# Kernel tuning notes

Hardware: AMD Instinct MI355X
Metric: run time of the kernel (lower is better)

## Reference

```python
import jax, jax.numpy as jnp
import numpy as np

WIDTH = 1024
NUM_HEADS = 8
POWER = 8.0
MIN_RAD, MAX_RAD = 0.9, 0.999


def setup_inputs() -> dict:
    key = jax.random.key(0)
    k_x, k_a, k_wi, k_wa = jax.random.split(key, 4)
    B, L, W, H = 4, 8192, WIDTH, NUM_HEADS
    bw = W // H
    x = jax.random.normal(k_x, (B, L, W), dtype=jnp.float32)
    # a_param init, matching RGLRU.__init__
    unif = jax.random.uniform(k_a, shape=(W,))
    a_real = 0.5 * jnp.log(unif * (MAX_RAD**2 - MIN_RAD**2) + MIN_RAD**2 + 1e-08)
    a_param = jnp.log(jnp.exp(-a_real) - 1.0)
    scale = jnp.sqrt(1.0 / bw).astype(jnp.float32)
    w_in = jax.random.normal(k_wi, (H, bw, bw), dtype=jnp.float32) * scale
    b_in = jnp.zeros((H, bw), dtype=jnp.float32)
    w_a = jax.random.normal(k_wa, (H, bw, bw), dtype=jnp.float32) * scale
    b_a = jnp.zeros((H, bw), dtype=jnp.float32)
    return {"x": x, "a_param": a_param, "w_in": w_in, "b_in": b_in,
            "w_a": w_a, "b_a": b_a}


def _block_diag_linear(x, w, b):
    # x: [B, L, W]; w: [H, bw, bw]; b: [H, bw]
    B, L, W = x.shape
    H, bw, _ = w.shape
    xh = x.reshape(B, L, H, bw)
    y = jnp.einsum('blhi,hij->blhj', xh, w) + b
    return y.reshape(B, L, W)


def reference(x, a_param, w_in, b_in, w_a, b_a):
    gate_x = jax.nn.sigmoid(_block_diag_linear(x, w_in, b_in))
    gate_a = jax.nn.sigmoid(_block_diag_linear(x, w_a, b_a))
    log_a = -POWER * gate_a * jax.nn.softplus(a_param)          # [B, L, W]
    a = jnp.exp(log_a)
    a_squared = jnp.exp(2.0 * log_a)
    normalized_x = x * gate_x * jnp.sqrt(1.0 - a_squared)        # [B, L, W]

    h0 = jnp.zeros_like(normalized_x[:, 0, :])                   # [B, W]

    def step(h, inp):
        a_t, x_t = inp                                           # [B, W] each
        h = a_t * h + x_t
        return h, h

    # scan over time axis: move L to leading dim
    _, ys = jax.lax.scan(step, h0,
                         (jnp.swapaxes(a, 0, 1), jnp.swapaxes(normalized_x, 0, 1)))
    return jnp.swapaxes(ys, 0, 1)                                # [B, L, W]
```

## Files before the change

kernel.cpp:

```cpp
#include <hip/hip_runtime.h>
#include <math.h>

#define NB 4
#define NL 8192
#define NW 1024
#define NH 8
#define BWID 128
#define POWERF 8.0f

#define TM 64
#define NRC (NL / TM)
#define NCHAIN (NB * NH)
#define NBLK (NRC * NCHAIN)

typedef __attribute__((ext_vector_type(8))) short bf16x8;
typedef __attribute__((ext_vector_type(8))) unsigned short u16x8;
typedef __attribute__((ext_vector_type(4))) float f32x4;

__device__ __forceinline__ unsigned short bf_hi(float f) {
  return (unsigned short)(__float_as_uint(f) >> 16);
}
__device__ __forceinline__ float bf_f(unsigned short h) {
  return __uint_as_float(((unsigned)h) << 16);
}

__global__ void prep_kernel(const float* __restrict__ w_in,
                            const float* __restrict__ w_a,
                            const float* __restrict__ a_param,
                            unsigned short* __restrict__ wt,
                            float* __restrict__ sp,
                            unsigned long long* __restrict__ hcarry,
                            int* __restrict__ ticket) {
  const int gtid = blockIdx.x * 256 + threadIdx.x;
  const int k   = gtid & 127;
  const int col = (gtid >> 7) & 127;
  const int hh  = (gtid >> 14) & 7;
  const int mat = gtid >> 17;
  const float* src = mat ? w_a : w_in;
  const float v = src[((size_t)hh * 128 + k) * 128 + col];
  const unsigned short hi = bf_hi(v);
  const unsigned short lo = bf_hi(v - bf_f(hi));
  wt[(((size_t)(mat * 2 + 0) * 8 + hh) * 128 + col) * 128 + k] = hi;
  wt[(((size_t)(mat * 2 + 1) * 8 + hh) * 128 + col) * 128 + k] = lo;
  if (gtid < NW) sp[gtid] = log1pf(expf(a_param[gtid]));
  const size_t ci = (size_t)gtid * 2;
  hcarry[ci] = 0ull;
  hcarry[ci + 1] = 0ull;
  if (gtid == 0) *ticket = 0;
}

__global__ __launch_bounds__(256, 3)
void fused_kernel(const float* __restrict__ x,
                  const unsigned short* __restrict__ wt,
                  const float* __restrict__ sp,
                  const float* __restrict__ b_in,
                  const float* __restrict__ b_a,
                  float* __restrict__ out,
                  int* __restrict__ ticket,
                  unsigned long long* __restrict__ hcarry) {
  __shared__ char smem[49152];
  char* const pXh = smem;
  char* const pXl = smem + 16384;
  char* const pW  = smem + 32768;
  char* const pSeg = smem + 32768;

  const int tid  = threadIdx.x;
  if (tid == 0) *(int*)smem = atomicAdd(ticket, 1);
  __syncthreads();
  const int vbid = *(const int*)smem;
  __syncthreads();
  const int rc = vbid >> 5;
  const int bh = vbid & 31;
  const int b  = bh >> 3;
  const int h  = bh & 7;

  const int lane = tid & 63;
  const int wid  = tid >> 6;
  const int g  = lane >> 4;
  const int ln = lane & 15;
  const int wr = wid >> 1;
  const int wc = wid & 1;

  const size_t xbase = ((size_t)b * NL + (size_t)rc * TM) * NW + h * BWID;

  int wsoff[4], wdoff[4];
#pragma unroll
  for (int i = 0; i < 4; ++i) {
    const int chunk = tid + 256 * i;
    const int split = chunk >> 9;
    const int rem = chunk & 511;
    const int col = rem >> 2;
    const int kk8 = (rem & 3) * 8;
    wsoff[i] = split * 131072 + h * 16384 + col * 128 + kk8;
    wdoff[i] = col * 128 + ((split * 64 + kk8 * 2) ^ ((col & 7) << 4));
  }
  u16x8 wreg[4];
#pragma unroll
  for (int i = 0; i < 4; ++i) wreg[i] = *(const u16x8*)(wt + wsoff[i]);

#pragma unroll
  for (int i = 0; i < 4; ++i) {
    const int chunk = tid + 256 * i;
    const int row = chunk >> 4;
    const int k8  = (chunk & 15) * 8;
    const float4 v0 = *(const float4*)(x + xbase + (size_t)row * NW + k8);
    const float4 v1 = *(const float4*)(x + xbase + (size_t)row * NW + k8 + 4);
    const float f[8] = {v0.x, v0.y, v0.z, v0.w, v1.x, v1.y, v1.z, v1.w};
    u16x8 vh, vl;
#pragma unroll
    for (int j = 0; j < 8; ++j) {
      const unsigned short hi = bf_hi(f[j]);
      vh[j] = hi;
      vl[j] = bf_hi(f[j] - bf_f(hi));
    }
    const int off = row * 256 + ((k8 * 2) ^ ((row & 15) << 4));
    *(u16x8*)(pXh + off) = vh;
    *(u16x8*)(pXl + off) = vl;
  }
  __syncthreads();
#pragma unroll
  for (int i = 0; i < 4; ++i) *(u16x8*)(pW + wdoff[i]) = wreg[i];
#pragma unroll
  for (int i = 0; i < 4; ++i)
    wreg[i] = *(const u16x8*)(wt + wsoff[i] + 262144);

  f32x4 accx[2][4], acca[2][4];
#pragma unroll
  for (int rt = 0; rt < 2; ++rt)
#pragma unroll
    for (int ct = 0; ct < 4; ++ct) {
      accx[rt][ct] = (f32x4){0.f, 0.f, 0.f, 0.f};
      acca[rt][ct] = (f32x4){0.f, 0.f, 0.f, 0.f};
    }

  const int csw = (ln & 7) << 4;
  const int gk  = g * 16;

#pragma unroll 1
  for (int j = 0; j < 4; ++j) {
    const int kt = j * 32;
    __syncthreads();
    bf16x8 Ah[2], Al[2];
#pragma unroll
    for (int rt = 0; rt < 2; ++rt) {
      const int arow = wr * 32 + rt * 16 + ln;
      const int abyte = arow * 256 + (((kt + g * 8) * 2) ^ ((arow & 15) << 4));
      Ah[rt] = *(const bf16x8*)(pXh + abyte);
      Al[rt] = *(const bf16x8*)(pXl + abyte);
    }
#pragma unroll
    for (int ct = 0; ct < 4; ++ct) {
      const int cb = (wc * 64 + ct * 16 + ln) * 128;
      const bf16x8 Bh = *(const bf16x8*)(pW + cb + ((gk) ^ csw));
      const bf16x8 Bl = *(const bf16x8*)(pW + cb + ((64 + gk) ^ csw));
#pragma unroll
      for (int rt = 0; rt < 2; ++rt) {
        accx[rt][ct] = __builtin_amdgcn_mfma_f32_16x16x32_bf16(Ah[rt], Bh, accx[rt][ct], 0, 0, 0);
        accx[rt][ct] = __builtin_amdgcn_mfma_f32_16x16x32_bf16(Al[rt], Bh, accx[rt][ct], 0, 0, 0);
        accx[rt][ct] = __builtin_amdgcn_mfma_f32_16x16x32_bf16(Ah[rt], Bl, accx[rt][ct], 0, 0, 0);
      }
    }
    __syncthreads();
#pragma unroll
    for (int i = 0; i < 4; ++i) *(u16x8*)(pW + wdoff[i]) = wreg[i];
    if (j < 3) {
#pragma unroll
      for (int i = 0; i < 4; ++i)
        wreg[i] = *(const u16x8*)(wt + wsoff[i] + kt + 32);
    }
    __syncthreads();
#pragma unroll
    for (int ct = 0; ct < 4; ++ct) {
      const int cb = (wc * 64 + ct * 16 + ln) * 128;
      const bf16x8 Bh = *(const bf16x8*)(pW + cb + ((gk) ^ csw));
      const bf16x8 Bl = *(const bf16x8*)(pW + cb + ((64 + gk) ^ csw));
#pragma unroll
      for (int rt = 0; rt < 2; ++rt) {
        acca[rt][ct] = __builtin_amdgcn_mfma_f32_16x16x32_bf16(Ah[rt], Bh, acca[rt][ct], 0, 0, 0);
        acca[rt][ct] = __builtin_amdgcn_mfma_f32_16x16x32_bf16(Al[rt], Bh, acca[rt][ct], 0, 0, 0);
        acca[rt][ct] = __builtin_amdgcn_mfma_f32_16x16x32_bf16(Ah[rt], Bl, acca[rt][ct], 0, 0, 0);
      }
    }
    __syncthreads();
    if (j < 3) {
#pragma unroll
      for (int i = 0; i < 4; ++i) *(u16x8*)(pW + wdoff[i]) = wreg[i];
#pragma unroll
      for (int i = 0; i < 4; ++i)
        wreg[i] = *(const u16x8*)(wt + wsoff[i] + 262144 + kt + 32);
    }
  }

  float av_sav[2][4][4], xn_sav[2][4][4];
#pragma unroll
  for (int ct = 0; ct < 4; ++ct) {
    const int col = wc * 64 + ct * 16 + ln;
    const float bi  = b_in[h * BWID + col];
    const float ba  = b_a[h * BWID + col];
    const float spv = sp[h * BWID + col];
#pragma unroll
    for (int rt = 0; rt < 2; ++rt) {
#pragma unroll
      for (int r = 0; r < 4; ++r) {
        const int row = wr * 32 + rt * 16 + g * 4 + r;
        const float zx = accx[rt][ct][r] + bi;
        const float za = acca[rt][ct][r] + ba;
        const int xoff = row * 256 + ((col * 2) ^ ((row & 15) << 4));
        const float xv = bf_f(*(const unsigned short*)(pXh + xoff)) +
                         bf_f(*(const unsigned short*)(pXl + xoff));
        const float gx = __builtin_amdgcn_rcpf(1.f + __expf(-zx));
        const float ga = __builtin_amdgcn_rcpf(1.f + __expf(-za));
        const float la = -POWERF * ga * spv;
        const float av = __expf(la);
        const float asq = __expf(2.f * la);
        av_sav[rt][ct][r] = av;
        xn_sav[rt][ct][r] = xv * gx * sqrtf(fmaxf(1.f - asq, 0.f));
      }
    }
  }

#pragma unroll
  for (int ct = 0; ct < 4; ++ct) {
    const int col = wc * 64 + ct * 16 + ln;
#pragma unroll
    for (int rt = 0; rt < 2; ++rt) {
      float A4 = 1.f, h4 = 0.f;
#pragma unroll
      for (int r = 0; r < 4; ++r) {
        h4 = fmaf(av_sav[rt][ct][r], h4, xn_sav[rt][ct][r]);
        A4 *= av_sav[rt][ct][r];
      }
      const int s = wr * 8 + rt * 4 + g;
      *(float2*)(pSeg + col * 128 + ((s * 8) ^ ((col & 15) << 3))) =
          make_float2(A4, h4);
    }
  }
  __syncthreads();

  if (tid < 128) {
    const int w = tid;
    float As[16], hs[16];
#pragma unroll
    for (int s = 0; s < 16; ++s) {
      const float2 v =
          *(const float2*)(pSeg + w * 128 + ((s * 8) ^ ((w & 15) << 3)));
      As[s] = v.x;
      hs[s] = v.y;
    }
    float hprev = 0.f;
    if (rc > 0) {
      const unsigned long long* srcw =
          hcarry + (size_t)(vbid - NCHAIN) * 128 + w;
      unsigned long long wv = __hip_atomic_load(srcw, __ATOMIC_RELAXED,
                                                __HIP_MEMORY_SCOPE_AGENT);
      int spins = 0;
      while ((wv >> 32) == 0ull) {
        __builtin_amdgcn_s_sleep(1);
        if (++spins > (1 << 18)) break;
        wv = __hip_atomic_load(srcw, __ATOMIC_RELAXED,
                               __HIP_MEMORY_SCOPE_AGENT);
      }
      hprev = __uint_as_float((unsigned)(wv & 0xffffffffull));
    }
    float p = hprev;
#pragma unroll
    for (int s = 0; s < 16; ++s) {
      *(float*)(pSeg + w * 128 + ((s * 8) ^ ((w & 15) << 3))) = p;
      p = fmaf(As[s], p, hs[s]);
    }
    __hip_atomic_store(hcarry + (size_t)vbid * 128 + w,
                       (1ull << 32) | (unsigned long long)__float_as_uint(p),
                       __ATOMIC_RELAXED, __HIP_MEMORY_SCOPE_AGENT);
  }
  __syncthreads();

#pragma unroll
  for (int ct = 0; ct < 4; ++ct) {
    const int col = wc * 64 + ct * 16 + ln;
#pragma unroll
    for (int rt = 0; rt < 2; ++rt) {
      const int s = wr * 8 + rt * 4 + g;
      float hh =
          *(const float*)(pSeg + col * 128 + ((s * 8) ^ ((col & 15) << 3)));
#pragma unroll
      for (int r = 0; r < 4; ++r) {
        hh = fmaf(av_sav[rt][ct][r], hh, xn_sav[rt][ct][r]);
        out[xbase + (size_t)(wr * 32 + rt * 16 + g * 4 + r) * NW + col] = hh;
      }
    }
  }
}

extern "C" void kernel_launch(void* const* d_in, const int* in_sizes, int n_in,
                              void* d_out, int out_size, void* d_ws, size_t ws_size,
                              hipStream_t stream) {
  const float* x       = (const float*)d_in[0];
  const float* a_param = (const float*)d_in[1];
  const float* w_in    = (const float*)d_in[2];
  const float* b_in    = (const float*)d_in[3];
  const float* w_a     = (const float*)d_in[4];
  const float* b_a     = (const float*)d_in[5];
  float* out = (float*)d_out;

  char* ws = (char*)d_ws;
  unsigned long long* hcarry = (unsigned long long*)ws;
  int* ticket = (int*)(ws + (4 << 20));
  unsigned short* wt = (unsigned short*)(ws + (4 << 20) + 1024);
  float* sp = (float*)(ws + (4 << 20) + 1024 + (1 << 20));

  prep_kernel<<<1024, 256, 0, stream>>>(w_in, w_a, a_param, wt, sp,
                                        hcarry, ticket);
  fused_kernel<<<NBLK, 256, 0, stream>>>(x, wt, sp, b_in, b_a, out,
                                         ticket, hcarry);
}
```

Baseline: 318.4 us.

## Use decoupled look-back for the cross-block recurrence carry

Each block now publishes its local segment aggregate (product of decay factors and the local scan value) before waiting on its predecessor. A waiting block walks back through earlier chunks, combining their published aggregates until it reaches an inclusive prefix, instead of spinning on the immediate predecessor alone. This targets the serial chain latency of the chained scan across 128 chunks. In exchange the carry buffer is doubled, the workspace offsets shift, and each block runs extra global atomic loads and a sign-bit flag encoding on the aggregate.

```diff
diff --git a/kernel.cpp b/kernel.cpp
--- a/kernel.cpp
+++ b/kernel.cpp
@@ -29,7 +29,7 @@
                             const float* __restrict__ a_param,
                             unsigned short* __restrict__ wt,
                             float* __restrict__ sp,
-                            unsigned long long* __restrict__ hcarry,
+                            unsigned long long* __restrict__ carry,
                             int* __restrict__ ticket) {
   const int gtid = blockIdx.x * 256 + threadIdx.x;
   const int k   = gtid & 127;
@@ -43,9 +43,11 @@
   wt[(((size_t)(mat * 2 + 0) * 8 + hh) * 128 + col) * 128 + k] = hi;
   wt[(((size_t)(mat * 2 + 1) * 8 + hh) * 128 + col) * 128 + k] = lo;
   if (gtid < NW) sp[gtid] = log1pf(expf(a_param[gtid]));
-  const size_t ci = (size_t)gtid * 2;
-  hcarry[ci] = 0ull;
-  hcarry[ci + 1] = 0ull;
+  const size_t ci = (size_t)gtid * 4;
+  carry[ci] = 0ull;
+  carry[ci + 1] = 0ull;
+  carry[ci + 2] = 0ull;
+  carry[ci + 3] = 0ull;
   if (gtid == 0) *ticket = 0;
 }
 
@@ -57,7 +59,7 @@
                   const float* __restrict__ b_a,
                   float* __restrict__ out,
                   int* __restrict__ ticket,
-                  unsigned long long* __restrict__ hcarry) {
+                  unsigned long long* __restrict__ carry) {
   __shared__ char smem[49152];
   char* const pXh = smem;
   char* const pXl = smem + 16384;
@@ -247,30 +249,57 @@
       As[s] = v.x;
       hs[s] = v.y;
     }
+    float Atot = 1.f, hloc = 0.f;
+#pragma unroll
+    for (int s = 0; s < 16; ++s) {
+      hloc = fmaf(As[s], hloc, hs[s]);
+      Atot *= As[s];
+    }
+    const size_t cbase = ((size_t)vbid * 128 + w) * 2;
+    __hip_atomic_store(carry + cbase + 1,
+                       ((unsigned long long)__float_as_uint(-Atot) << 32) |
+                           (unsigned long long)__float_as_uint(hloc),
+                       __ATOMIC_RELAXED, __HIP_MEMORY_SCOPE_AGENT);
+
     float hprev = 0.f;
     if (rc > 0) {
-      const unsigned long long* srcw =
-          hcarry + (size_t)(vbid - NCHAIN) * 128 + w;
-      unsigned long long wv = __hip_atomic_load(srcw, __ATOMIC_RELAXED,
-                                                __HIP_MEMORY_SCOPE_AGENT);
+      float P = 1.f, q = 0.f;
+      int j = vbid - NCHAIN;
       int spins = 0;
-      while ((wv >> 32) == 0ull) {
+      while (true) {
+        const size_t jb = ((size_t)j * 128 + w) * 2;
+        const unsigned long long wi = __hip_atomic_load(
+            carry + jb, __ATOMIC_RELAXED, __HIP_MEMORY_SCOPE_AGENT);
+        if (wi >> 32) {
+          hprev = fmaf(P, __uint_as_float((unsigned)wi), q);
+          break;
+        }
+        const unsigned long long wl = __hip_atomic_load(
+            carry + jb + 1, __ATOMIC_RELAXED, __HIP_MEMORY_SCOPE_AGENT);
+        if (wl >> 63) {
+          const float Aj = -__uint_as_float((unsigned)(wl >> 32));
+          const float hj = __uint_as_float((unsigned)wl);
+          q = fmaf(P, hj, q);
+          P *= Aj;
+          if (j < NCHAIN) { hprev = q; break; }
+          j -= NCHAIN;
+          continue;
+        }
         __builtin_amdgcn_s_sleep(1);
-        if (++spins > (1 << 18)) break;
-        wv = __hip_atomic_load(srcw, __ATOMIC_RELAXED,
-                               __HIP_MEMORY_SCOPE_AGENT);
-      }
-      hprev = __uint_as_float((unsigned)(wv & 0xffffffffull));
-    }
+        if (++spins > (1 << 18)) { hprev = q; break; }
+      }
+    }
+    const float Hm = fmaf(Atot, hprev, hloc);
+    __hip_atomic_store(carry + cbase,
+                       (1ull << 32) | (unsigned long long)__float_as_uint(Hm),
+                       __ATOMIC_RELAXED, __HIP_MEMORY_SCOPE_AGENT);
+
     float p = hprev;
 #pragma unroll
     for (int s = 0; s < 16; ++s) {
       *(float*)(pSeg + w * 128 + ((s * 8) ^ ((w & 15) << 3))) = p;
       p = fmaf(As[s], p, hs[s]);
     }
-    __hip_atomic_store(hcarry + (size_t)vbid * 128 + w,
-                       (1ull << 32) | (unsigned long long)__float_as_uint(p),
-                       __ATOMIC_RELAXED, __HIP_MEMORY_SCOPE_AGENT);
   }
   __syncthreads();
 
@@ -303,13 +332,13 @@
   float* out = (float*)d_out;
 
   char* ws = (char*)d_ws;
-  unsigned long long* hcarry = (unsigned long long*)ws;
-  int* ticket = (int*)(ws + (4 << 20));
-  unsigned short* wt = (unsigned short*)(ws + (4 << 20) + 1024);
-  float* sp = (float*)(ws + (4 << 20) + 1024 + (1 << 20));
+  unsigned long long* carry = (unsigned long long*)ws;
+  int* ticket = (int*)(ws + (8 << 20));
+  unsigned short* wt = (unsigned short*)(ws + (8 << 20) + 1024);
+  float* sp = (float*)(ws + (8 << 20) + 1024 + (1 << 20));
 
   prep_kernel<<<1024, 256, 0, stream>>>(w_in, w_a, a_param, wt, sp,
-                                        hcarry, ticket);
+                                        carry, ticket);
   fused_kernel<<<NBLK, 256, 0, stream>>>(x, wt, sp, b_in, b_a, out,
-                                         ticket, hcarry);
-}
+                                         ticket, carry);
+}
```

Measured after the change: 299.0 us. 1.06x faster.
